# Performance work log

Hardware: AMD Instinct MI355X
Metric: run time of the kernel (lower is better)

## Reference

```python
import jax, jax.numpy as jnp
import numpy as np

B, S, H, DK = 2, 2048, 16, 64
D = H * DK  # d_model = 1024


def setup_inputs() -> dict:
    key = jax.random.key(0)
    ks = jax.random.split(key, 12)
    inp = {
        "queries": jax.random.normal(ks[0], (B, S, D), jnp.float32),
        "keys": jax.random.normal(ks[1], (B, S, D), jnp.float32),
        "values": jax.random.normal(ks[2], (B, S, D), jnp.float32),
        # additive 0/1 mask (1 = masked out), causal upper-triangular
        "mask": jnp.triu(jnp.ones((S, S), jnp.float32), k=1)[None, None, :, :],
        "W_q": jax.random.normal(ks[3], (D, D), jnp.float32) / np.sqrt(D),
        "b_q": jnp.zeros((D,), jnp.float32),
        "W_k": jax.random.normal(ks[4], (D, D), jnp.float32) / np.sqrt(D),
        "b_k": jnp.zeros((D,), jnp.float32),
        "W_v": jax.random.normal(ks[5], (D, D), jnp.float32) / np.sqrt(D),
        "b_v": jnp.zeros((D,), jnp.float32),
        "W_o": jax.random.normal(ks[6], (D, D), jnp.float32) / np.sqrt(D),
        "b_o": jnp.zeros((D,), jnp.float32),
    }
    return inp


def _split_heads(x):
    # (B, S, D) -> (B, H, S, DK)
    return x.reshape(x.shape[0], x.shape[1], H, DK).transpose(0, 2, 1, 3)


def reference(queries, keys, values, mask, W_q, b_q, W_k, b_k, W_v, b_v, W_o, b_o):
    q = _split_heads(queries @ W_q + b_q)  # (B, H, S, DK)
    k = _split_heads(keys @ W_k + b_k)
    v = _split_heads(values @ W_v + b_v)
    scale = 1.0 / jnp.sqrt(jnp.asarray(DK, q.dtype))
    scores = jnp.einsum("bhqd,bhkd->bhqk", q, k) * scale  # (B, H, S, S)
    scores = scores + (-1e9) * mask
    weights = jax.nn.softmax(scores, axis=-1)
    o = jnp.einsum("bhqk,bhkd->bhqd", weights, v)  # (B, H, S, DK)
    o = o.transpose(0, 2, 1, 3).reshape(queries.shape[0], queries.shape[1], D)
    return o @ W_o + b_o
```

## Files before the change

kernel.cpp:

```cpp
#include <hip/hip_runtime.h>
#include <hip/hip_bf16.h>
#include <stdint.h>

typedef unsigned short u16;
typedef __attribute__((ext_vector_type(4))) float f32x4;
typedef __attribute__((ext_vector_type(8))) short bf16x8;

#define B_ 2
#define S_ 2048
#define H_ 16
#define D_ 1024
#define XELEMS (B_*S_*D_)
#define WELEMS (D_*D_)
#define QSCALE 0.18033688f

__device__ __forceinline__ u16 f2bf(float f) {
  union { float f; unsigned u; } v; v.f = f;
  unsigned r = v.u + 0x7fffu + ((v.u >> 16) & 1u);
  return (u16)(r >> 16);
}

__device__ __forceinline__ void async16(const void* g, void* l) {
  __builtin_amdgcn_global_load_lds(
      (const __attribute__((address_space(1))) unsigned int*)g,
      (__attribute__((address_space(3))) unsigned int*)l, 16, 0, 0);
}

#if __has_builtin(__builtin_amdgcn_exp2f)
#define EXP2(x) __builtin_amdgcn_exp2f(x)
#else
#define EXP2(x) exp2f(x)
#endif

__device__ __forceinline__ unsigned cvtpk(float a, float b) {
  unsigned r;
  asm("v_cvt_pk_bf16_f32 %0, %1, %2" : "=v"(r) : "v"(a), "v"(b));
  return r;
}

__global__ __launch_bounds__(256) void prep_k(
    const float* __restrict__ q, const float* __restrict__ k,
    const float* __restrict__ v,
    const float* __restrict__ Wq, const float* __restrict__ Wk,
    const float* __restrict__ Wv, const float* __restrict__ Wo,
    u16* __restrict__ X, u16* __restrict__ WT) {
  const int bid = blockIdx.x;
  if (bid < 4096) {
    __shared__ float tile[32][33];
    const int z = bid >> 10, rem = bid & 1023;
    const float* W = (z == 0) ? Wq : (z == 1) ? Wk : (z == 2) ? Wv : Wo;
    u16* o = WT + z * WELEMS;
    const int r0 = (rem >> 5) << 5, c0 = (rem & 31) << 5;
    const int tx = threadIdx.x & 31, ty = threadIdx.x >> 5;
    #pragma unroll
    for (int rr = ty; rr < 32; rr += 8)
      tile[rr][tx] = W[(r0 + rr) * D_ + c0 + tx];
    __syncthreads();
    #pragma unroll
    for (int rr = ty; rr < 32; rr += 8)
      o[(c0 + rr) * D_ + r0 + tx] = f2bf(tile[tx][rr]);
  } else {
    const int cb = bid - 4096;
    const int ngrp = XELEMS / 8;
    const int total = 3 * ngrp;
    for (int i = cb * 256 + threadIdx.x; i < total; i += 1024 * 256) {
      int which = i / ngrp;
      int off = (i - which * ngrp) * 8;
      const float* src = (which == 0) ? q : (which == 1) ? k : v;
      float4 a = *(const float4*)(src + off);
      float4 b = *(const float4*)(src + off + 4);
      u16 rr[8] = {f2bf(a.x), f2bf(a.y), f2bf(a.z), f2bf(a.w),
                   f2bf(b.x), f2bf(b.y), f2bf(b.z), f2bf(b.w)};
      uint4 pk;
      pk.x = (unsigned)rr[0] | ((unsigned)rr[1] << 16);
      pk.y = (unsigned)rr[2] | ((unsigned)rr[3] << 16);
      pk.z = (unsigned)rr[4] | ((unsigned)rr[5] << 16);
      pk.w = (unsigned)rr[6] | ((unsigned)rr[7] << 16);
      *(uint4*)(X + which * XELEMS + off) = pk;
    }
  }
}

template <int MODE, int DBUF>
__device__ __forceinline__ void gemm_body(const u16* __restrict__ A,
                                          const u16* __restrict__ BT,
                                          const float* __restrict__ bias,
                                          void* __restrict__ outp,
                                          int bm, int bn, float scale) {
  constexpr int SMEM_BYTES = DBUF ? 65536 : ((MODE == 0 || MODE == 2) ? 34816 : 32768);
  __shared__ __align__(16) char smem[SMEM_BYTES];
  const int tid = threadIdx.x;
  const int w = tid >> 6, l = tid & 63;
  const int wr = w >> 1, wc = w & 1;
  const int g = l >> 4, r = l & 15;
  (void)w; (void)l;

  f32x4 acc[4][4];
  #pragma unroll
  for (int i = 0; i < 4; i++)
    #pragma unroll
    for (int j = 0; j < 4; j++) acc[i][j] = (f32x4){0.f, 0.f, 0.f, 0.f};

  int dst[4], aoff[4], boff[4];
  #pragma unroll
  for (int i = 0; i < 4; i++) {
    const int o = i * 4096 + tid * 16;
    dst[i] = o;
    const int row = o >> 7;
    const int cbyte = (o & 127) ^ ((row & 7) << 4);
    aoff[i] = (bm + row) * 1024 + (cbyte >> 1);
    boff[i] = (bn + row) * 1024 + (cbyte >> 1);
  }

  if (DBUF == 0) {
    char* Ab = smem;
    char* Bb = smem + 16384;
    for (int t = 0; t < 16; ++t) {
      const int k0 = t * 64;
      #pragma unroll
      for (int i = 0; i < 4; i++) async16(A + aoff[i] + k0, Ab + dst[i]);
      #pragma unroll
      for (int i = 0; i < 4; i++) async16(BT + boff[i] + k0, Bb + dst[i]);
      __syncthreads();
      bf16x8 af[2][4], bf[2][4];
      #pragma unroll
      for (int kk = 0; kk < 2; kk++)
        #pragma unroll
        for (int mi = 0; mi < 4; mi++) {
          const int rA = wr * 64 + mi * 16 + r;
          af[kk][mi] = *(const bf16x8*)(Ab +
              ((rA * 128 + kk * 64 + g * 16) ^ ((rA & 7) << 4)));
        }
      #pragma unroll
      for (int kk = 0; kk < 2; kk++)
        #pragma unroll
        for (int ni = 0; ni < 4; ni++) {
          const int rB = wc * 64 + ni * 16 + r;
          bf[kk][ni] = *(const bf16x8*)(Bb +
              ((rB * 128 + kk * 64 + g * 16) ^ ((rB & 7) << 4)));
        }
      #pragma unroll
      for (int kk = 0; kk < 2; kk++)
        #pragma unroll
        for (int mi = 0; mi < 4; mi++)
          #pragma unroll
          for (int ni = 0; ni < 4; ni++)
            acc[mi][ni] = __builtin_amdgcn_mfma_f32_16x16x32_bf16(
                af[kk][mi], bf[kk][ni], acc[mi][ni], 0, 0, 0);
      __syncthreads();
    }
  } else {
    #pragma unroll
    for (int i = 0; i < 4; i++) {
      async16(A + aoff[i], smem + dst[i]);
      async16(BT + boff[i], smem + 16384 + dst[i]);
    }
    for (int t = 0; t < 16; ++t) {
      const int buf = t & 1;
      const char* Ab = smem + buf * 32768;
      const char* Bb = Ab + 16384;
      if (t < 15) {
        const int k0 = (t + 1) * 64;
        char* An = smem + (buf ^ 1) * 32768;
        #pragma unroll
        for (int i = 0; i < 4; i++) {
          async16(A + aoff[i] + k0, An + dst[i]);
          async16(BT + boff[i] + k0, An + 16384 + dst[i]);
        }
        asm volatile("s_waitcnt vmcnt(8)" ::: "memory");
      } else {
        asm volatile("s_waitcnt vmcnt(0)" ::: "memory");
      }
      asm volatile("s_barrier" ::: "memory");

      bf16x8 af[2][4], bf[2][4];
      #pragma unroll
      for (int kk = 0; kk < 2; kk++)
        #pragma unroll
        for (int mi = 0; mi < 4; mi++) {
          const int rA = wr * 64 + mi * 16 + r;
          af[kk][mi] = *(const bf16x8*)(Ab +
              ((rA * 128 + kk * 64 + g * 16) ^ ((rA & 7) << 4)));
        }
      #pragma unroll
      for (int kk = 0; kk < 2; kk++)
        #pragma unroll
        for (int ni = 0; ni < 4; ni++) {
          const int rB = wc * 64 + ni * 16 + r;
          bf[kk][ni] = *(const bf16x8*)(Bb +
              ((rB * 128 + kk * 64 + g * 16) ^ ((rB & 7) << 4)));
        }
      __builtin_amdgcn_s_setprio(1);
      #pragma unroll
      for (int kk = 0; kk < 2; kk++)
        #pragma unroll
        for (int mi = 0; mi < 4; mi++)
          #pragma unroll
          for (int ni = 0; ni < 4; ni++)
            acc[mi][ni] = __builtin_amdgcn_mfma_f32_16x16x32_bf16(
                af[kk][mi], bf[kk][ni], acc[mi][ni], 0, 0, 0);
      __builtin_amdgcn_s_setprio(0);
      asm volatile("s_barrier" ::: "memory");
    }
  }

  const int col0 = bn + wc * 64;
  float bc[4];
  #pragma unroll
  for (int ni = 0; ni < 4; ni++) bc[ni] = bias[col0 + ni * 16 + r];

  if (MODE == 0) {
    u16* Ts = (u16*)smem;
    #pragma unroll
    for (int mi = 0; mi < 4; mi++) {
      #pragma unroll
      for (int ni = 0; ni < 4; ni++) {
        const int lcol = wc * 64 + ni * 16 + r;
        #pragma unroll
        for (int i = 0; i < 4; i++) {
          const int lrow = wr * 64 + mi * 16 + g * 4 + i;
          Ts[lrow * 136 + lcol] = f2bf((acc[mi][ni][i] + bc[ni]) * scale);
        }
      }
    }
    __syncthreads();
    u16* out = (u16*)outp;
    const int bb = bm >> 11;
    const int sbase = bm & 2047;
    #pragma unroll
    for (int j = 0; j < 8; j++) {
      const int c = j * 256 + tid;
      const int row = c >> 4, oct = c & 15;
      const int col = bn + oct * 8;
      const int h = col >> 6, dk = col & 63;
      bf16x8 vv = *(const bf16x8*)&Ts[row * 136 + oct * 8];
      *(bf16x8*)&out[(((size_t)((bb << 4) | h) * 2048 + sbase + row) << 6) + dk] = vv;
    }
  } else if (MODE == 2) {
    u16* Ts = (u16*)smem;
    #pragma unroll
    for (int mi = 0; mi < 4; mi++) {
      const int lrow = wr * 64 + mi * 16 + g * 4;
      #pragma unroll
      for (int ni = 0; ni < 4; ni++) {
        const int lcol = wc * 64 + ni * 16 + r;
        u16 p0 = f2bf(acc[mi][ni][0] + bc[ni]);
        u16 p1 = f2bf(acc[mi][ni][1] + bc[ni]);
        u16 p2 = f2bf(acc[mi][ni][2] + bc[ni]);
        u16 p3 = f2bf(acc[mi][ni][3] + bc[ni]);
        uint2 pk;
        pk.x = (unsigned)p0 | ((unsigned)p1 << 16);
        pk.y = (unsigned)p2 | ((unsigned)p3 << 16);
        *(uint2*)&Ts[lcol * 136 + lrow] = pk;
      }
    }
    __syncthreads();
    u16* out = (u16*)outp;
    const int bb = bm >> 11;
    const int sbase = bm & 2047;
    #pragma unroll
    for (int j = 0; j < 8; j++) {
      const int c = (tid >> 6) * 512 + j * 64 + (tid & 63);
      const int dk = c >> 4, sc = c & 15;
      const int col = bn + dk;
      const int h = col >> 6, dkk = col & 63;
      bf16x8 vv = *(const bf16x8*)&Ts[dk * 136 + sc * 8];
      *(bf16x8*)&out[(((size_t)(((bb << 4) | h) * 64 + dkk)) << 11) +
                     sbase + sc * 8] = vv;
    }
  } else {
    float* out = (float*)outp;
    #pragma unroll
    for (int mi = 0; mi < 4; mi++) {
      const int row = bm + wr * 64 + mi * 16 + g * 4;
      #pragma unroll
      for (int ni = 0; ni < 4; ni++) {
        const int col = col0 + ni * 16 + r;
        #pragma unroll
        for (int i = 0; i < 4; i++)
          out[(row + i) * 1024 + col] = acc[mi][ni][i] + bc[ni];
      }
    }
  }
}

__global__ __launch_bounds__(256) void gemm_qkv_k(
    const u16* __restrict__ X, const u16* __restrict__ WT,
    const float* __restrict__ bq, const float* __restrict__ bk,
    const float* __restrict__ bv, u16* __restrict__ QKV) {
  const int z = blockIdx.z;
  const float* bias = (z == 0) ? bq : (z == 1) ? bk : bv;
  if (z == 2)
    gemm_body<2, 0>(X + z * XELEMS, WT + z * WELEMS, bias, QKV + z * XELEMS,
                    blockIdx.x * 128, blockIdx.y * 128, 1.0f);
  else
    gemm_body<0, 0>(X + z * XELEMS, WT + z * WELEMS, bias, QKV + z * XELEMS,
                    blockIdx.x * 128, blockIdx.y * 128,
                    (z == 0) ? QSCALE : 1.0f);
}

__global__ __launch_bounds__(256) void gemm_o_k(
    const u16* __restrict__ O, const u16* __restrict__ WOT,
    const float* __restrict__ bo, float* __restrict__ out) {
  gemm_body<1, 1>(O, WOT, bo, out, blockIdx.x * 128, blockIdx.y * 128, 1.0f);
}

__global__ __launch_bounds__(512) void attn_k(
    const u16* __restrict__ Qh, const u16* __restrict__ Kh,
    const u16* __restrict__ VTh, u16* __restrict__ O) {
  __shared__ __align__(16) char ldsK[3][8192];
  __shared__ __align__(16) char ldsV[3][8192];
  __shared__ __align__(16) u16 ldsP[8][16 * 72];

  const int bh = blockIdx.y;
  const int pj = blockIdx.x;
  const int tid = threadIdx.x;
  const int w = tid >> 6, l = tid & 63;
  const int grp = w >> 2, wg = w & 3;
  const int g = l >> 4, r = l & 15;
  const int b = bh >> 4, h = bh & 15;

  const u16* Qp = Qh + bh * (S_ * 64);
  const char* Kp = (const char*)(Kh + bh * (S_ * 64));
  const char* Vp = (const char*)(VTh + bh * (64 * S_));

  const int o = w * 1024 + l * 16;
  const int kdst = o;
  const int ksrc = o ^ (((o >> 7) & 7) << 4);
  const int vd = o >> 7, vcb = o & 127;
  const int vfix = vd * (S_ * 2) + (vcb ^ ((vd & 7) << 4));
  u16* Pq = &ldsP[w][0];

  const int qt = grp ? (31 - pj) : pj;
  const int q0w = qt * 64 + wg * 16;
  const int my_nt = qt + 1;
  const int nt_max = 32 - pj;
  const int qloc = wg * 16 + r;

  bf16x8 qf[2];
  #pragma unroll
  for (int dh = 0; dh < 2; dh++)
    qf[dh] = *(const bf16x8*)(Qp + (q0w + r) * 64 + dh * 32 + g * 8);
  asm volatile("s_waitcnt vmcnt(0)" ::: "memory");

  f32x4 accT[4];
  #pragma unroll
  for (int dn = 0; dn < 4; dn++) accT[dn] = (f32x4){0.f, 0.f, 0.f, 0.f};
  float mrun = -1e30f, lsum = 0.f;

  async16(Kp + ksrc, &ldsK[0][0] + kdst);
  async16(Vp + vfix, &ldsV[0][0] + kdst);
  async16(Kp + 8192 + ksrc, &ldsK[1][0] + kdst);
  async16(Vp + 128 + vfix, &ldsV[1][0] + kdst);

  int cur = 0, pre = 2;
  for (int t = 0; t < nt_max; ++t) {
    if (t + 2 < nt_max) {
      async16(Kp + (t + 2) * 8192 + ksrc, &ldsK[pre][0] + kdst);
      async16(Vp + (t + 2) * 128 + vfix, &ldsV[pre][0] + kdst);
      asm volatile("s_waitcnt vmcnt(4)" ::: "memory");
    } else if (t + 1 < nt_max) {
      asm volatile("s_waitcnt vmcnt(2)" ::: "memory");
    } else {
      asm volatile("s_waitcnt vmcnt(0)" ::: "memory");
    }
    asm volatile("s_barrier" ::: "memory");

    if (t < my_nt) {
      const char* Kb = &ldsK[cur][0];
      f32x4 sc[4];
      #pragma unroll
      for (int ct = 0; ct < 4; ct++) {
        const int row = ct * 16 + r;
        const int sw = (row & 7) << 4;
        bf16x8 k0 = *(const bf16x8*)(Kb + ((row * 128 + g * 16) ^ sw));
        bf16x8 k1 = *(const bf16x8*)(Kb + ((row * 128 + 64 + g * 16) ^ sw));
        f32x4 z = (f32x4){0.f, 0.f, 0.f, 0.f};
        z = __builtin_amdgcn_mfma_f32_16x16x32_bf16(k0, qf[0], z, 0, 0, 0);
        sc[ct] = __builtin_amdgcn_mfma_f32_16x16x32_bf16(k1, qf[1], z, 0, 0, 0);
      }

      if (t == my_nt - 1) {
        #pragma unroll
        for (int ct = 0; ct < 4; ct++)
          #pragma unroll
          for (int i = 0; i < 4; i++)
            if (ct * 16 + g * 4 + i > qloc) sc[ct][i] = -1e9f;
      }

      float a0 = fmaxf(fmaxf(sc[0][0], sc[0][1]), sc[0][2]);
      float a1 = fmaxf(fmaxf(sc[0][3], sc[1][0]), sc[1][1]);
      float a2 = fmaxf(fmaxf(sc[1][2], sc[1][3]), sc[2][0]);
      float a3 = fmaxf(fmaxf(sc[2][1], sc[2][2]), sc[2][3]);
      float a4 = fmaxf(fmaxf(sc[3][0], sc[3][1]), sc[3][2]);
      float pmax = fmaxf(fmaxf(fmaxf(a0, a1), fmaxf(a2, a3)),
                         fmaxf(a4, sc[3][3]));
      pmax = fmaxf(pmax, __shfl_xor(pmax, 16, 64));
      pmax = fmaxf(pmax, __shfl_xor(pmax, 32, 64));

      if (!__all(pmax - mrun <= 11.0f)) {
        const float mnew = fmaxf(mrun, pmax);
        const float corr = EXP2(mrun - mnew);
        mrun = mnew;
        #pragma unroll
        for (int dn = 0; dn < 4; dn++)
          #pragma unroll
          for (int i = 0; i < 4; i++) accT[dn][i] *= corr;
        lsum *= corr;
      }

      float ps = 0.f;
      #pragma unroll
      for (int ct = 0; ct < 4; ct++)
        #pragma unroll
        for (int i = 0; i < 4; i++) {
          const float p = EXP2(sc[ct][i] - mrun);
          sc[ct][i] = p;
          ps += p;
        }
      ps += __shfl_xor(ps, 16, 64);
      ps += __shfl_xor(ps, 32, 64);
      lsum += ps;

      #pragma unroll
      for (int ct = 0; ct < 4; ct++) {
        uint2 pk;
        pk.x = cvtpk(sc[ct][0], sc[ct][1]);
        pk.y = cvtpk(sc[ct][2], sc[ct][3]);
        *(uint2*)&Pq[r * 72 + ct * 16 + g * 4] = pk;
      }
      asm volatile("s_waitcnt lgkmcnt(0)" ::: "memory");

      const char* Vb = &ldsV[cur][0];
      bf16x8 pf[2];
      #pragma unroll
      for (int kp = 0; kp < 2; kp++)
        pf[kp] = *(const bf16x8*)&Pq[r * 72 + kp * 32 + g * 8];
      __builtin_amdgcn_s_setprio(1);
      #pragma unroll
      for (int dn = 0; dn < 4; dn++) {
        const int vrow = dn * 16 + r;
        const int vsw = (vrow & 7) << 4;
        #pragma unroll
        for (int kp = 0; kp < 2; kp++) {
          bf16x8 vf = *(const bf16x8*)(Vb + ((vrow * 128 + kp * 64 + g * 16) ^ vsw));
          accT[dn] = __builtin_amdgcn_mfma_f32_16x16x32_bf16(vf, pf[kp], accT[dn], 0, 0, 0);
        }
      }
      __builtin_amdgcn_s_setprio(0);
    }
    asm volatile("s_barrier" ::: "memory");
    cur = (cur == 2) ? 0 : cur + 1;
    pre = (pre == 2) ? 0 : pre + 1;
  }

  const float inv = 1.0f / lsum;
  const int qrow = q0w + r;
  #pragma unroll
  for (int dn = 0; dn < 4; dn++) {
    u16 o0 = f2bf(accT[dn][0] * inv), o1 = f2bf(accT[dn][1] * inv);
    u16 o2 = f2bf(accT[dn][2] * inv), o3 = f2bf(accT[dn][3] * inv);
    uint2 pk;
    pk.x = (unsigned)o0 | ((unsigned)o1 << 16);
    pk.y = (unsigned)o2 | ((unsigned)o3 << 16);
    *(uint2*)(O + ((size_t)(b * 2048 + qrow)) * 1024 + h * 64 + dn * 16 + g * 4) = pk;
  }
}

extern "C" void kernel_launch(void* const* d_in, const int* in_sizes, int n_in,
                              void* d_out, int out_size, void* d_ws, size_t ws_size,
                              hipStream_t stream) {
  const float* q  = (const float*)d_in[0];
  const float* k  = (const float*)d_in[1];
  const float* v  = (const float*)d_in[2];
  const float* Wq = (const float*)d_in[4];
  const float* bq = (const float*)d_in[5];
  const float* Wk = (const float*)d_in[6];
  const float* bk = (const float*)d_in[7];
  const float* Wv = (const float*)d_in[8];
  const float* bv = (const float*)d_in[9];
  const float* Wo = (const float*)d_in[10];
  const float* bo = (const float*)d_in[11];

  char* ws = (char*)d_ws;
  const size_t MB = 1u << 20;
  u16* X   = (u16*)(ws);
  u16* WT  = (u16*)(ws + 24 * MB);
  u16* QKV = (u16*)(ws + 32 * MB);
  u16* O   = (u16*)(ws);

  hipLaunchKernelGGL(prep_k, dim3(5120), dim3(256), 0, stream,
                     q, k, v, Wq, Wk, Wv, Wo, X, WT);
  hipLaunchKernelGGL(gemm_qkv_k, dim3(32, 8, 3), dim3(256), 0, stream,
                     X, WT, bq, bk, bv, QKV);
  hipLaunchKernelGGL(attn_k, dim3(16, 32), dim3(512), 0, stream,
                     QKV, QKV + XELEMS, QKV + 2 * XELEMS, O);
  hipLaunchKernelGGL(gemm_o_k, dim3(32, 8), dim3(256), 0, stream,
                     O, WT + 3 * WELEMS, bo, (float*)d_out);
}
```

Baseline: 128.2 us.

## Split attention KV range across two wave groups per query tile, merge softmax states

Each attention block now handles a single 64-row query tile, and its two 4-wave groups take alternating KV tiles (a split-K style split) instead of pairing a short and a long query tile. Partial max, sum and accumulators are merged through LDS at the end. Blocks are launched heaviest-first, and the grid doubles to 32x32. The P staging buffer shrinks by writing and reading P in two halves, and KV buffering becomes a double-buffered pair of tiles per round. This is meant to improve load balance and parallelism, at the cost of an LDS merge step and more waitcnt serialization in the PV stage.

```diff
diff --git a/kernel.cpp b/kernel.cpp
--- a/kernel.cpp
+++ b/kernel.cpp
@@ -308,15 +308,15 @@
 __global__ __launch_bounds__(512) void attn_k(
     const u16* __restrict__ Qh, const u16* __restrict__ Kh,
     const u16* __restrict__ VTh, u16* __restrict__ O) {
-  __shared__ __align__(16) char ldsK[3][8192];
-  __shared__ __align__(16) char ldsV[3][8192];
-  __shared__ __align__(16) u16 ldsP[8][16 * 72];
+  __shared__ __align__(16) char ldsK[2][2][8192];
+  __shared__ __align__(16) char ldsV[2][2][8192];
+  __shared__ __align__(16) u16 ldsP[8][16 * 40];
 
   const int bh = blockIdx.y;
-  const int pj = blockIdx.x;
+  const int pj = 31 - (int)blockIdx.x;
   const int tid = threadIdx.x;
   const int w = tid >> 6, l = tid & 63;
-  const int grp = w >> 2, wg = w & 3;
+  const int g2 = w >> 2, wg = w & 3;
   const int g = l >> 4, r = l & 15;
   const int b = bh >> 4, h = bh & 15;
 
@@ -331,10 +331,8 @@
   const int vfix = vd * (S_ * 2) + (vcb ^ ((vd & 7) << 4));
   u16* Pq = &ldsP[w][0];
 
-  const int qt = grp ? (31 - pj) : pj;
-  const int q0w = qt * 64 + wg * 16;
-  const int my_nt = qt + 1;
-  const int nt_max = 32 - pj;
+  const int rounds = (pj >> 1) + 1;
+  const int q0w = pj * 64 + wg * 16;
   const int qloc = wg * 16 + r;
 
   bf16x8 qf[2];
@@ -348,26 +346,29 @@
   for (int dn = 0; dn < 4; dn++) accT[dn] = (f32x4){0.f, 0.f, 0.f, 0.f};
   float mrun = -1e30f, lsum = 0.f;
 
-  async16(Kp + ksrc, &ldsK[0][0] + kdst);
-  async16(Vp + vfix, &ldsV[0][0] + kdst);
-  async16(Kp + 8192 + ksrc, &ldsK[1][0] + kdst);
-  async16(Vp + 128 + vfix, &ldsV[1][0] + kdst);
-
-  int cur = 0, pre = 2;
-  for (int t = 0; t < nt_max; ++t) {
-    if (t + 2 < nt_max) {
-      async16(Kp + (t + 2) * 8192 + ksrc, &ldsK[pre][0] + kdst);
-      async16(Vp + (t + 2) * 128 + vfix, &ldsV[pre][0] + kdst);
+  async16(Kp + ksrc, &ldsK[0][0][0] + kdst);
+  async16(Kp + 8192 + ksrc, &ldsK[0][1][0] + kdst);
+  async16(Vp + vfix, &ldsV[0][0][0] + kdst);
+  async16(Vp + 128 + vfix, &ldsV[0][1][0] + kdst);
+
+  for (int u = 0; u < rounds; ++u) {
+    const int pr = u & 1;
+    if (u + 1 < rounds) {
+      int ta = 2 * u + 2; if (ta > 31) ta = 31;
+      int tb = 2 * u + 3; if (tb > 31) tb = 31;
+      async16(Kp + ta * 8192 + ksrc, &ldsK[pr ^ 1][0][0] + kdst);
+      async16(Kp + tb * 8192 + ksrc, &ldsK[pr ^ 1][1][0] + kdst);
+      async16(Vp + ta * 128 + vfix, &ldsV[pr ^ 1][0][0] + kdst);
+      async16(Vp + tb * 128 + vfix, &ldsV[pr ^ 1][1][0] + kdst);
       asm volatile("s_waitcnt vmcnt(4)" ::: "memory");
-    } else if (t + 1 < nt_max) {
-      asm volatile("s_waitcnt vmcnt(2)" ::: "memory");
     } else {
       asm volatile("s_waitcnt vmcnt(0)" ::: "memory");
     }
     asm volatile("s_barrier" ::: "memory");
 
-    if (t < my_nt) {
-      const char* Kb = &ldsK[cur][0];
+    const int tt = 2 * u + g2;
+    if (tt <= pj) {
+      const char* Kb = &ldsK[pr][g2][0];
       f32x4 sc[4];
       #pragma unroll
       for (int ct = 0; ct < 4; ct++) {
@@ -380,7 +381,7 @@
         sc[ct] = __builtin_amdgcn_mfma_f32_16x16x32_bf16(k1, qf[1], z, 0, 0, 0);
       }
 
-      if (t == my_nt - 1) {
+      if (tt == pj) {
         #pragma unroll
         for (int ct = 0; ct < 4; ct++)
           #pragma unroll
@@ -422,48 +423,78 @@
       ps += __shfl_xor(ps, 32, 64);
       lsum += ps;
 
-      #pragma unroll
-      for (int ct = 0; ct < 4; ct++) {
-        uint2 pk;
-        pk.x = cvtpk(sc[ct][0], sc[ct][1]);
-        pk.y = cvtpk(sc[ct][2], sc[ct][3]);
-        *(uint2*)&Pq[r * 72 + ct * 16 + g * 4] = pk;
+      const char* Vb = &ldsV[pr][g2][0];
+      {
+        uint2 pk0, pk1;
+        pk0.x = cvtpk(sc[0][0], sc[0][1]); pk0.y = cvtpk(sc[0][2], sc[0][3]);
+        pk1.x = cvtpk(sc[1][0], sc[1][1]); pk1.y = cvtpk(sc[1][2], sc[1][3]);
+        *(uint2*)&Pq[r * 40 + g * 4] = pk0;
+        *(uint2*)&Pq[r * 40 + 16 + g * 4] = pk1;
       }
       asm volatile("s_waitcnt lgkmcnt(0)" ::: "memory");
-
-      const char* Vb = &ldsV[cur][0];
-      bf16x8 pf[2];
-      #pragma unroll
-      for (int kp = 0; kp < 2; kp++)
-        pf[kp] = *(const bf16x8*)&Pq[r * 72 + kp * 32 + g * 8];
+      bf16x8 pf0 = *(const bf16x8*)&Pq[r * 40 + g * 8];
+      asm volatile("s_waitcnt lgkmcnt(0)" ::: "memory");
+      {
+        uint2 pk2, pk3;
+        pk2.x = cvtpk(sc[2][0], sc[2][1]); pk2.y = cvtpk(sc[2][2], sc[2][3]);
+        pk3.x = cvtpk(sc[3][0], sc[3][1]); pk3.y = cvtpk(sc[3][2], sc[3][3]);
+        *(uint2*)&Pq[r * 40 + g * 4] = pk2;
+        *(uint2*)&Pq[r * 40 + 16 + g * 4] = pk3;
+      }
       __builtin_amdgcn_s_setprio(1);
       #pragma unroll
       for (int dn = 0; dn < 4; dn++) {
         const int vrow = dn * 16 + r;
         const int vsw = (vrow & 7) << 4;
-        #pragma unroll
-        for (int kp = 0; kp < 2; kp++) {
-          bf16x8 vf = *(const bf16x8*)(Vb + ((vrow * 128 + kp * 64 + g * 16) ^ vsw));
-          accT[dn] = __builtin_amdgcn_mfma_f32_16x16x32_bf16(vf, pf[kp], accT[dn], 0, 0, 0);
-        }
+        bf16x8 vf = *(const bf16x8*)(Vb + ((vrow * 128 + g * 16) ^ vsw));
+        accT[dn] = __builtin_amdgcn_mfma_f32_16x16x32_bf16(vf, pf0, accT[dn], 0, 0, 0);
       }
       __builtin_amdgcn_s_setprio(0);
+      asm volatile("s_waitcnt lgkmcnt(0)" ::: "memory");
+      bf16x8 pf1 = *(const bf16x8*)&Pq[r * 40 + g * 8];
+      __builtin_amdgcn_s_setprio(1);
+      #pragma unroll
+      for (int dn = 0; dn < 4; dn++) {
+        const int vrow = dn * 16 + r;
+        const int vsw = (vrow & 7) << 4;
+        bf16x8 vf = *(const bf16x8*)(Vb + ((vrow * 128 + 64 + g * 16) ^ vsw));
+        accT[dn] = __builtin_amdgcn_mfma_f32_16x16x32_bf16(vf, pf1, accT[dn], 0, 0, 0);
+      }
+      __builtin_amdgcn_s_setprio(0);
     }
     asm volatile("s_barrier" ::: "memory");
-    cur = (cur == 2) ? 0 : cur + 1;
-    pre = (pre == 2) ? 0 : pre + 1;
-  }
-
-  const float inv = 1.0f / lsum;
-  const int qrow = q0w + r;
-  #pragma unroll
-  for (int dn = 0; dn < 4; dn++) {
-    u16 o0 = f2bf(accT[dn][0] * inv), o1 = f2bf(accT[dn][1] * inv);
-    u16 o2 = f2bf(accT[dn][2] * inv), o3 = f2bf(accT[dn][3] * inv);
-    uint2 pk;
-    pk.x = (unsigned)o0 | ((unsigned)o1 << 16);
-    pk.y = (unsigned)o2 | ((unsigned)o3 << 16);
-    *(uint2*)(O + ((size_t)(b * 2048 + qrow)) * 1024 + h * 64 + dn * 16 + g * 4) = pk;
+  }
+
+  float* scr = (float*)&ldsK[0][0][0];
+  if (w >= 4) {
+    float* dst = scr + (size_t)(w - 4) * 1280 + l * 20;
+    dst[0] = mrun; dst[1] = lsum;
+    #pragma unroll
+    for (int dn = 0; dn < 4; dn++)
+      *(f32x4*)(dst + 4 + dn * 4) = accT[dn];
+  }
+  __syncthreads();
+  if (w < 4) {
+    const float* src = scr + (size_t)w * 1280 + l * 20;
+    const float mo = src[0], lo = src[1];
+    const float ms = fmaxf(mrun, mo);
+    const float cE = EXP2(mrun - ms);
+    const float cO = EXP2(mo - ms);
+    const float li = lsum * cE + lo * cO;
+    const float inv = 1.0f / li;
+    const int qrow = q0w + r;
+    #pragma unroll
+    for (int dn = 0; dn < 4; dn++) {
+      f32x4 ao = *(const f32x4*)(src + 4 + dn * 4);
+      float v0 = (accT[dn][0] * cE + ao[0] * cO) * inv;
+      float v1 = (accT[dn][1] * cE + ao[1] * cO) * inv;
+      float v2 = (accT[dn][2] * cE + ao[2] * cO) * inv;
+      float v3 = (accT[dn][3] * cE + ao[3] * cO) * inv;
+      uint2 pk;
+      pk.x = (unsigned)f2bf(v0) | ((unsigned)f2bf(v1) << 16);
+      pk.y = (unsigned)f2bf(v2) | ((unsigned)f2bf(v3) << 16);
+      *(uint2*)(O + ((size_t)(b * 2048 + qrow)) * 1024 + h * 64 + dn * 16 + g * 4) = pk;
+    }
   }
 }
 
@@ -493,7 +524,7 @@
                      q, k, v, Wq, Wk, Wv, Wo, X, WT);
   hipLaunchKernelGGL(gemm_qkv_k, dim3(32, 8, 3), dim3(256), 0, stream,
                      X, WT, bq, bk, bv, QKV);
-  hipLaunchKernelGGL(attn_k, dim3(16, 32), dim3(512), 0, stream,
+  hipLaunchKernelGGL(attn_k, dim3(32, 32), dim3(512), 0, stream,
                      QKV, QKV + XELEMS, QKV + 2 * XELEMS, O);
   hipLaunchKernelGGL(gemm_o_k, dim3(32, 8), dim3(256), 0, stream,
                      O, WT + 3 * WELEMS, bo, (float*)d_out);
```

Result: slower. 142.0 us (+10.7%).
